# Kernel optimization log

Measured on AMD Instinct MI355X. Metric: run time of the kernel, lower is better.

The kernel has to match this reference:

```python
import jax, jax.numpy as jnp
from jax import lax
import numpy as np
import math

D = 256; H = 4; DH = 64; PERIOD = 30; WIN = 4; L = 2
AUDIO = 768; MOTION = 33
B = 8; T = 1024; S = 1024


def _pe_table(t, d=D, period=PERIOD):
    pos = np.arange(period, dtype=np.float32)[:, None]
    div = np.exp(np.arange(0, d, 2, dtype=np.float32) * (-math.log(10000.0) / d))
    pe = np.zeros((period, d), np.float32)
    pe[:, 0::2] = np.sin(pos * div)
    pe[:, 1::2] = np.cos(pos * div)
    reps = t // period + 1
    return jnp.asarray(np.tile(pe, (reps, 1))[:t])


def _tgt_mask(t):
    # ALiBi-style bias (quantized by period) + causal mask, per head. [H,t,t]
    slopes = jnp.array([0.25 ** (i + 1) for i in range(H)], jnp.float32)
    i = jnp.arange(t)[:, None]
    j = jnp.arange(t)[None, :]
    rel = i - j
    alibi = jnp.where(rel >= 0, -(rel // PERIOD).astype(jnp.float32), 0.0)
    causal = jnp.where(rel >= 0, 0.0, -jnp.inf)
    return slopes[:, None, None] * alibi + causal[None]


def _mem_mask(t, s):
    i = jnp.arange(t)[:, None]
    j = jnp.arange(s)[None, :]
    return jnp.where(jnp.abs(i - j) <= WIN, 0.0, -jnp.inf)


def _ln(x, g, b, eps=1e-5):
    mu = jnp.mean(x, -1, keepdims=True)
    var = jnp.mean(jnp.square(x - mu), -1, keepdims=True)
    return (x - mu) * lax.rsqrt(var + eps) * g + b


def _mha(xq, xkv, in_w, in_b, out_w, out_b, mask):
    wq, wk, wv = jnp.split(in_w, 3, axis=0)
    bq, bk, bv = jnp.split(in_b, 3)
    q = xq @ wq.T + bq
    k = xkv @ wk.T + bk
    v = xkv @ wv.T + bv
    b_, t_, _ = q.shape
    s_ = k.shape[1]
    q = q.reshape(b_, t_, H, DH)
    k = k.reshape(b_, s_, H, DH)
    v = v.reshape(b_, s_, H, DH)
    scores = jnp.einsum('bthd,bshd->bhts', q, k) / math.sqrt(DH) + mask
    a = jax.nn.softmax(scores, axis=-1)
    o = jnp.einsum('bhts,bshd->bthd', a, v).reshape(b_, t_, D)
    return o @ out_w.T + out_b


def _conv1d(x_nch, w, b):
    y = lax.conv_general_dilated(x_nch, w, (1,), [(2, 2)],
                                 dimension_numbers=('NCH', 'OIH', 'NCH'))
    return y + b[None, :, None]


def setup_inputs() -> dict:
    key = jax.random.key(0)
    ks = iter(jax.random.split(key, 40))

    def r(shape, s=0.05):
        return jax.random.normal(next(ks), shape, jnp.float32) * s

    return {
        'hidden_states': jax.random.normal(next(ks), (B, S, AUDIO), jnp.float32),
        'target_motions': jax.random.uniform(next(ks), (B, T, MOTION), jnp.float32),
        'W_af': r((D, AUDIO)), 'b_af': r((D,)),
        'conv1_w': r((D, D, 5)), 'conv1_b': r((D,)),
        'conv2_w': r((D, D, 5)), 'conv2_b': r((D,)),
        'W_vm': r((D, MOTION)), 'b_vm': r((D,)),
        'sa_in_w': r((L, 3 * D, D)), 'sa_in_b': r((L, 3 * D)),
        'sa_out_w': r((L, D, D)), 'sa_out_b': r((L, D)),
        'ca_in_w': r((L, 3 * D, D)), 'ca_in_b': r((L, 3 * D)),
        'ca_out_w': r((L, D, D)), 'ca_out_b': r((L, D)),
        'ln1_g': jnp.ones((L, D)), 'ln1_b': jnp.zeros((L, D)),
        'ln2_g': jnp.ones((L, D)), 'ln2_b': jnp.zeros((L, D)),
        'ln3_g': jnp.ones((L, D)), 'ln3_b': jnp.zeros((L, D)),
        'ff1_w': r((L, 2 * D, D)), 'ff1_b': r((L, 2 * D)),
        'ff2_w': r((L, D, 2 * D)), 'ff2_b': r((L, D)),
        'W_vr': r((MOTION, D)), 'b_vr': r((MOTION,)),
    }


def reference(hidden_states, target_motions, W_af, b_af, conv1_w, conv1_b,
              conv2_w, conv2_b, W_vm, b_vm, sa_in_w, sa_in_b, sa_out_w,
              sa_out_b, ca_in_w, ca_in_b, ca_out_w, ca_out_b, ln1_g, ln1_b,
              ln2_g, ln2_b, ln3_g, ln3_b, ff1_w, ff1_b, ff2_w, ff2_b,
              W_vr, b_vr):
    # audio encoder: linear + residual temporal convs (exact GELU)
    audio = hidden_states @ W_af.T + b_af                       # [B,S,D]
    c = _conv1d(audio.transpose(0, 2, 1), conv1_w, conv1_b)
    c = jax.nn.gelu(c, approximate=False)
    c = _conv1d(c, conv2_w, conv2_b)
    audio = audio + c.transpose(0, 2, 1)

    b_, t_, _ = target_motions.shape
    motion_in = jnp.concatenate(
        [jnp.zeros((b_, 1, MOTION), target_motions.dtype),
         target_motions[:, :-1]], axis=1)
    x = motion_in @ W_vm.T + b_vm + _pe_table(t_)               # PPE (eval: no dropout)

    tm = _tgt_mask(t_)                                          # [H,t,t]
    mm = _mem_mask(t_, audio.shape[1])                          # [t,s]

    for l in range(L):  # post-norm TransformerDecoderLayer, relu FFN
        x = _ln(x + _mha(x, x, sa_in_w[l], sa_in_b[l], sa_out_w[l], sa_out_b[l], tm),
                ln1_g[l], ln1_b[l])
        x = _ln(x + _mha(x, audio, ca_in_w[l], ca_in_b[l], ca_out_w[l], ca_out_b[l], mm),
                ln2_g[l], ln2_b[l])
        h = jax.nn.relu(x @ ff1_w[l].T + ff1_b[l]) @ ff2_w[l].T + ff2_b[l]
        x = _ln(x + h, ln3_g[l], ln3_b[l])

    return jnp.clip(x @ W_vr.T + b_vr, 0.0, 1.0)
```

## Files before the change

kernel.cpp:

```cpp
#include <hip/hip_runtime.h>
#include <math.h>

#define B_ 8
#define T_ 1024
#define S_ 1024
#define D_ 256
#define H_ 4
#define DH_ 64
#define AUDIO_ 768
#define MOTION_ 33
#define PERIOD_ 30
#define WIN_ 4
#define M_ (B_ * T_)

typedef _Float16 half8 __attribute__((ext_vector_type(8)));
typedef _Float16 half4 __attribute__((ext_vector_type(4)));
typedef __attribute__((ext_vector_type(4))) float f32x4;

#define O_AF    0
#define O_SAIN  196608
#define O_SAOUT 589824
#define O_CAIN  720896
#define O_CAOUT 1114112
#define O_FF1   1245184
#define O_FF2   1507328
#define O_CONV1 1769472
#define O_CONV2 2097152
#define O_VR    2424832
#define WH_TOT  2441216
#define HID_TOT 6291456

struct CvtSrc { const float* p[17]; };

__global__ __launch_bounds__(256) void cvt_all(
    CvtSrc s, _Float16* __restrict__ wH, _Float16* __restrict__ hidH) {
  const long i = (long)blockIdx.x * 256 + threadIdx.x;
  if (i >= (long)WH_TOT + HID_TOT) return;
  if (i >= WH_TOT) { const long j = i - WH_TOT; hidH[j] = (_Float16)s.p[15][j]; return; }
  if (i >= O_VR) {
    const long j = i - O_VR, oc = j >> 8, cin = j & 255;
    wH[i] = (oc < MOTION_) ? (_Float16)s.p[16][oc * 256 + cin] : (_Float16)0.f;
    return;
  }
  if (i >= O_CONV2) {
    const long j = i - O_CONV2, oc = j / 1280, r = j % 1280, tap = r >> 8, cin = r & 255;
    wH[i] = (_Float16)s.p[14][(oc * 256 + cin) * 5 + tap]; return;
  }
  if (i >= O_CONV1) {
    const long j = i - O_CONV1, oc = j / 1280, r = j % 1280, tap = r >> 8, cin = r & 255;
    wH[i] = (_Float16)s.p[13][(oc * 256 + cin) * 5 + tap]; return;
  }
  int seg; long base;
  if      (i >= 1638400) { seg = 12; base = 1638400; }
  else if (i >= 1507328) { seg = 11; base = 1507328; }
  else if (i >= 1376256) { seg = 10; base = 1376256; }
  else if (i >= 1245184) { seg = 9;  base = 1245184; }
  else if (i >= 1179648) { seg = 8;  base = 1179648; }
  else if (i >= 1114112) { seg = 7;  base = 1114112; }
  else if (i >= 917504)  { seg = 6;  base = 917504; }
  else if (i >= 720896)  { seg = 5;  base = 720896; }
  else if (i >= 655360)  { seg = 4;  base = 655360; }
  else if (i >= 589824)  { seg = 3;  base = 589824; }
  else if (i >= 393216)  { seg = 2;  base = 393216; }
  else if (i >= 196608)  { seg = 1;  base = 196608; }
  else                   { seg = 0;  base = 0; }
  wH[i] = (_Float16)s.p[seg][i - base];
}

__global__ __launch_bounds__(256) void gemm_h(
    const _Float16* __restrict__ A, const _Float16* __restrict__ W,
    const float* __restrict__ bias, float* __restrict__ Cf,
    _Float16* __restrict__ Ch, int M, int N, int K, int relu) {
  __shared__ _Float16 As[64][72];
  __shared__ _Float16 Bs[64][72];
  const int tid = threadIdx.x;
  const int wave = tid >> 6, lane = tid & 63;
  const int wr = wave >> 1, wc = wave & 1;
  const int lr16 = lane & 15, kq = lane >> 4;
  const int bm = blockIdx.x, bn = blockIdx.y;
  const int sr = tid >> 2, sq = tid & 3;

  const _Float16* Ap = A + (size_t)(bm * 64 + sr) * K + sq * 8;
  const _Float16* Wp = W + (size_t)(bn * 64 + sr) * K + sq * 8;

  half8 ra0 = *reinterpret_cast<const half8*>(Ap);
  half8 ra1 = *reinterpret_cast<const half8*>(Ap + 32);
  half8 rw0 = *reinterpret_cast<const half8*>(Wp);
  half8 rw1 = *reinterpret_cast<const half8*>(Wp + 32);
  f32x4 acc[2][2] = {};

  for (int k0 = 0; k0 < K; k0 += 64) {
    __syncthreads();
    *reinterpret_cast<half8*>(&As[sr][sq * 8]) = ra0;
    *reinterpret_cast<half8*>(&As[sr][32 + sq * 8]) = ra1;
    *reinterpret_cast<half8*>(&Bs[sr][sq * 8]) = rw0;
    *reinterpret_cast<half8*>(&Bs[sr][32 + sq * 8]) = rw1;
    __syncthreads();
    if (k0 + 64 < K) {
      ra0 = *reinterpret_cast<const half8*>(Ap + k0 + 64);
      ra1 = *reinterpret_cast<const half8*>(Ap + k0 + 96);
      rw0 = *reinterpret_cast<const half8*>(Wp + k0 + 64);
      rw1 = *reinterpret_cast<const half8*>(Wp + k0 + 96);
    }
    half8 af[2][2], bf[2][2];
#pragma unroll
    for (int m = 0; m < 2; ++m)
#pragma unroll
      for (int s = 0; s < 2; ++s)
        af[m][s] = *reinterpret_cast<const half8*>(
            &As[wr * 32 + m * 16 + lr16][s * 32 + kq * 8]);
#pragma unroll
    for (int n = 0; n < 2; ++n)
#pragma unroll
      for (int s = 0; s < 2; ++s)
        bf[n][s] = *reinterpret_cast<const half8*>(
            &Bs[wc * 32 + n * 16 + lr16][s * 32 + kq * 8]);
#pragma unroll
    for (int m = 0; m < 2; ++m)
#pragma unroll
      for (int n = 0; n < 2; ++n)
#pragma unroll
        for (int s = 0; s < 2; ++s)
          acc[m][n] = __builtin_amdgcn_mfma_f32_16x16x32_f16(af[m][s], bf[n][s], acc[m][n], 0, 0, 0);
  }

#pragma unroll
  for (int m = 0; m < 2; ++m) {
#pragma unroll
    for (int n = 0; n < 2; ++n) {
      const int col = bn * 64 + wc * 32 + n * 16 + lr16;
      const float bv = bias[col];
#pragma unroll
      for (int j = 0; j < 4; ++j) {
        const int row = bm * 64 + wr * 32 + m * 16 + kq * 4 + j;
        float v = acc[m][n][j] + bv;
        if (relu) v = fmaxf(v, 0.f);
        const size_t idx = (size_t)row * N + col;
        if (Cf) Cf[idx] = v;
        if (Ch) Ch[idx] = (_Float16)v;
      }
    }
  }
}

__device__ __forceinline__ half8 conv_ld(const _Float16* Xb, int p, int tap, int cin) {
  const int sp = p + tap - 2;
  if (sp < 0 || sp >= S_) { half8 z = {}; return z; }
  return *reinterpret_cast<const half8*>(Xb + (size_t)sp * D_ + cin);
}

__global__ __launch_bounds__(256) void conv_h(
    const _Float16* __restrict__ Xh, const _Float16* __restrict__ Wc,
    const float* __restrict__ bias, _Float16* __restrict__ OutH,
    const float* __restrict__ ResF, int mode) {
  __shared__ _Float16 As[64][72];
  __shared__ _Float16 Bs[64][72];
  const int tid = threadIdx.x;
  const int wave = tid >> 6, lane = tid & 63;
  const int wr = wave >> 1, wc = wave & 1;
  const int lr16 = lane & 15, kq = lane >> 4;
  const int b = blockIdx.x >> 4;
  const int s0 = (blockIdx.x & 15) * 64;
  const int o0 = blockIdx.y * 64;
  const int sr = tid >> 2, sq = tid & 3;

  const _Float16* Xb = Xh + (size_t)b * S_ * D_;
  const _Float16* Wp = Wc + (size_t)(o0 + sr) * 1280 + sq * 8;
  const int p = s0 + sr;

  half8 ra0 = conv_ld(Xb, p, 0, sq * 8);
  half8 ra1 = conv_ld(Xb, p, 0, 32 + sq * 8);
  half8 rw0 = *reinterpret_cast<const half8*>(Wp);
  half8 rw1 = *reinterpret_cast<const half8*>(Wp + 32);
  f32x4 acc[2][2] = {};

  for (int k0 = 0; k0 < 1280; k0 += 64) {
    __syncthreads();
    *reinterpret_cast<half8*>(&As[sr][sq * 8]) = ra0;
    *reinterpret_cast<half8*>(&As[sr][32 + sq * 8]) = ra1;
    *reinterpret_cast<half8*>(&Bs[sr][sq * 8]) = rw0;
    *reinterpret_cast<half8*>(&Bs[sr][32 + sq * 8]) = rw1;
    __syncthreads();
    if (k0 + 64 < 1280) {
      const int kn = k0 + 64;
      const int tap = kn >> 8, cb = kn & 255;
      ra0 = conv_ld(Xb, p, tap, cb + sq * 8);
      ra1 = conv_ld(Xb, p, tap, cb + 32 + sq * 8);
      rw0 = *reinterpret_cast<const half8*>(Wp + kn);
      rw1 = *reinterpret_cast<const half8*>(Wp + kn + 32);
    }
    half8 af[2][2], bf[2][2];
#pragma unroll
    for (int m = 0; m < 2; ++m)
#pragma unroll
      for (int s = 0; s < 2; ++s)
        af[m][s] = *reinterpret_cast<const half8*>(
            &As[wr * 32 + m * 16 + lr16][s * 32 + kq * 8]);
#pragma unroll
    for (int n = 0; n < 2; ++n)
#pragma unroll
      for (int s = 0; s < 2; ++s)
        bf[n][s] = *reinterpret_cast<const half8*>(
            &Bs[wc * 32 + n * 16 + lr16][s * 32 + kq * 8]);
#pragma unroll
    for (int m = 0; m < 2; ++m)
#pragma unroll
      for (int n = 0; n < 2; ++n)
#pragma unroll
        for (int s = 0; s < 2; ++s)
          acc[m][n] = __builtin_amdgcn_mfma_f32_16x16x32_f16(af[m][s], bf[n][s], acc[m][n], 0, 0, 0);
  }

#pragma unroll
  for (int m = 0; m < 2; ++m) {
#pragma unroll
    for (int n = 0; n < 2; ++n) {
      const int oc = o0 + wc * 32 + n * 16 + lr16;
      const float bv = bias[oc];
#pragma unroll
      for (int j = 0; j < 4; ++j) {
        const int s = s0 + wr * 32 + m * 16 + kq * 4 + j;
        const size_t idx = ((size_t)b * S_ + s) * D_ + oc;
        float v = acc[m][n][j] + bv;
        if (mode == 0) {
          v = 0.5f * v * (1.f + erff(v * 0.70710678118654752f));
        } else {
          v += ResF[idx];
        }
        OutH[idx] = (_Float16)v;
      }
    }
  }
}

__global__ __launch_bounds__(256) void head_mfma(
    const _Float16* __restrict__ Xh, const _Float16* __restrict__ Wh,
    const float* __restrict__ bv, float* __restrict__ Out) {
  __shared__ _Float16 As[64][72];
  __shared__ _Float16 Bs[64][72];
  const int tid = threadIdx.x;
  const int wave = tid >> 6, lane = tid & 63;
  const int wr = wave >> 1, wc = wave & 1;
  const int lr16 = lane & 15, kq = lane >> 4;
  const int bm = blockIdx.x;
  const int sr = tid >> 2, sq = tid & 3;

  const _Float16* Ap = Xh + (size_t)(bm * 64 + sr) * D_ + sq * 8;
  const _Float16* Wp = Wh + (size_t)sr * D_ + sq * 8;

  half8 ra0 = *reinterpret_cast<const half8*>(Ap);
  half8 ra1 = *reinterpret_cast<const half8*>(Ap + 32);
  half8 rw0 = *reinterpret_cast<const half8*>(Wp);
  half8 rw1 = *reinterpret_cast<const half8*>(Wp + 32);
  f32x4 acc[2][2] = {};

  for (int k0 = 0; k0 < D_; k0 += 64) {
    __syncthreads();
    *reinterpret_cast<half8*>(&As[sr][sq * 8]) = ra0;
    *reinterpret_cast<half8*>(&As[sr][32 + sq * 8]) = ra1;
    *reinterpret_cast<half8*>(&Bs[sr][sq * 8]) = rw0;
    *reinterpret_cast<half8*>(&Bs[sr][32 + sq * 8]) = rw1;
    __syncthreads();
    if (k0 + 64 < D_) {
      ra0 = *reinterpret_cast<const half8*>(Ap + k0 + 64);
      ra1 = *reinterpret_cast<const half8*>(Ap + k0 + 96);
      rw0 = *reinterpret_cast<const half8*>(Wp + k0 + 64);
      rw1 = *reinterpret_cast<const half8*>(Wp + k0 + 96);
    }
    half8 af[2][2], bf[2][2];
#pragma unroll
    for (int m = 0; m < 2; ++m)
#pragma unroll
      for (int s = 0; s < 2; ++s)
        af[m][s] = *reinterpret_cast<const half8*>(
            &As[wr * 32 + m * 16 + lr16][s * 32 + kq * 8]);
#pragma unroll
    for (int n = 0; n < 2; ++n)
#pragma unroll
      for (int s = 0; s < 2; ++s)
        bf[n][s] = *reinterpret_cast<const half8*>(
            &Bs[wc * 32 + n * 16 + lr16][s * 32 + kq * 8]);
#pragma unroll
    for (int m = 0; m < 2; ++m)
#pragma unroll
      for (int n = 0; n < 2; ++n)
#pragma unroll
        for (int s = 0; s < 2; ++s)
          acc[m][n] = __builtin_amdgcn_mfma_f32_16x16x32_f16(af[m][s], bf[n][s], acc[m][n], 0, 0, 0);
  }

#pragma unroll
  for (int m = 0; m < 2; ++m) {
#pragma unroll
    for (int n = 0; n < 2; ++n) {
      const int col = wc * 32 + n * 16 + lr16;
      if (col < MOTION_) {
        const float bb = bv[col];
#pragma unroll
        for (int j = 0; j < 4; ++j) {
          const int row = bm * 64 + wr * 32 + m * 16 + kq * 4 + j;
          float v = acc[m][n][j] + bb;
          Out[(size_t)row * MOTION_ + col] = fminf(fmaxf(v, 0.f), 1.f);
        }
      }
    }
  }
}

__global__ __launch_bounds__(256) void motion_pe(
    const float* __restrict__ TM, const float* __restrict__ Wvm,
    const float* __restrict__ bvm, float* __restrict__ Xout,
    _Float16* __restrict__ XoutH) {
  const int d = threadIdx.x;
  const int bt = blockIdx.x;
  const int t = bt & (T_ - 1);
  const int b = bt >> 10;
  float acc = bvm[d];
  if (t > 0) {
    const float* mrow = TM + ((size_t)b * T_ + t - 1) * MOTION_;
    const float* wrow = Wvm + (size_t)d * MOTION_;
#pragma unroll
    for (int m = 0; m < MOTION_; ++m) acc += mrow[m] * wrow[m];
  }
  const int pos = t % PERIOD_;
  const int i2 = d >> 1;
  const float div = expf((float)(2 * i2) * (-9.210340371976184f / 256.f));
  const float ang = (float)pos * div;
  acc += (d & 1) ? cosf(ang) : sinf(ang);
  Xout[(size_t)bt * D_ + d] = acc;
  XoutH[(size_t)bt * D_ + d] = (_Float16)acc;
}

#define RS_ 72
__global__ __launch_bounds__(512) void self_attn(
    const _Float16* __restrict__ QKV, _Float16* __restrict__ O) {
  __shared__ _Float16 Ks[64 * RS_];
  __shared__ _Float16 VTs[64 * RS_];
  __shared__ _Float16 Ps[8][16 * RS_];
  const int qtb = blockIdx.x, h = blockIdx.y, b = blockIdx.z;
  const int tid = threadIdx.x;
  const int wave = tid >> 6, lane = tid & 63;
  const int lo = lane & 15, hi = lane >> 4;
  const float slope = exp2f(-2.f * (float)(h + 1));
  const int qloc = wave * 16 + lo;
  const int tq = qtb * 128 + qloc;
  const size_t base = (size_t)b * T_ * 768 + h * 64;

  half8 qf[2];
#pragma unroll
  for (int s = 0; s < 2; ++s)
    qf[s] = *reinterpret_cast<const half8*>(
        QKV + base + (size_t)(qtb * 128 + qloc) * 768 + s * 32 + hi * 8);

  f32x4 oacc[4] = {};
  float mrun = -1e30f, lrun = 0.f;

  const int nkt = 2 * qtb + 2;
  for (int kt = 0; kt < nkt; ++kt) {
    __syncthreads();
    {
      const int j = tid >> 3, ch = tid & 7;
      const size_t rowoff = base + (size_t)(kt * 64 + j) * 768;
      *reinterpret_cast<half8*>(&Ks[j * RS_ + ch * 8]) =
          *reinterpret_cast<const half8*>(QKV + rowoff + 256 + ch * 8);
      const half8 vv = *reinterpret_cast<const half8*>(QKV + rowoff + 512 + ch * 8);
#pragma unroll
      for (int r = 0; r < 8; ++r) {
        const int d = ch * 8 + r;
        const int sw = ((d & 7) ^ (d >> 3)) << 3;
        VTs[d * RS_ + (j ^ sw)] = vv[r];
      }
    }
    __syncthreads();

    f32x4 st[4] = {};
#pragma unroll
    for (int f = 0; f < 4; ++f) {
#pragma unroll
      for (int s = 0; s < 2; ++s) {
        const half8 kf = *reinterpret_cast<const half8*>(
            &Ks[(f * 16 + lo) * RS_ + s * 32 + hi * 8]);
        st[f] = __builtin_amdgcn_mfma_f32_16x16x32_f16(kf, qf[s], st[f], 0, 0, 0);
      }
    }

    float sc[4][4];
    float tmax = -1e30f;
#pragma unroll
    for (int f = 0; f < 4; ++f)
#pragma unroll
      for (int r = 0; r < 4; ++r) {
        const int j = kt * 64 + f * 16 + hi * 4 + r;
        const int rel = tq - j;
        const float v = (rel >= 0)
            ? st[f][r] * 0.125f - slope * (float)(rel / PERIOD_) : -1e30f;
        sc[f][r] = v;
        tmax = fmaxf(tmax, v);
      }
    tmax = fmaxf(tmax, __shfl_xor(tmax, 16, 64));
    tmax = fmaxf(tmax, __shfl_xor(tmax, 32, 64));
    const float mnew = fmaxf(mrun, tmax);
    const float scale = __expf(mrun - mnew);

    float psum = 0.f;
#pragma unroll
    for (int f = 0; f < 4; ++f) {
      half4 ph;
#pragma unroll
      for (int r = 0; r < 4; ++r) {
        const float pv = __expf(sc[f][r] - mnew);
        psum += pv;
        ph[r] = (_Float16)pv;
      }
      *reinterpret_cast<half4*>(&Ps[wave][lo * RS_ + f * 16 + hi * 4]) = ph;
    }
    psum += __shfl_xor(psum, 16, 64);
    psum += __shfl_xor(psum, 32, 64);
    lrun = lrun * scale + psum;
    mrun = mnew;

    float rsc[4];
#pragma unroll
    for (int r = 0; r < 4; ++r) rsc[r] = __shfl(scale, hi * 4 + r, 64);
#pragma unroll
    for (int nf = 0; nf < 4; ++nf)
#pragma unroll
      for (int r = 0; r < 4; ++r) oacc[nf][r] *= rsc[r];

#pragma unroll
    for (int s = 0; s < 2; ++s) {
      const half8 pf = *reinterpret_cast<const half8*>(
          &Ps[wave][lo * RS_ + s * 32 + hi * 8]);
#pragma unroll
      for (int nf = 0; nf < 4; ++nf) {
        const int d = nf * 16 + lo;
        const int sw = ((d & 7) ^ (d >> 3)) << 3;
        const half8 vf = *reinterpret_cast<const half8*>(
            &VTs[d * RS_ + ((s * 32 + hi * 8) ^ sw)]);
        oacc[nf] = __builtin_amdgcn_mfma_f32_16x16x32_f16(pf, vf, oacc[nf], 0, 0, 0);
      }
    }
  }

  float invl[4];
#pragma unroll
  for (int r = 0; r < 4; ++r) invl[r] = 1.f / __shfl(lrun, hi * 4 + r, 64);
#pragma unroll
  for (int nf = 0; nf < 4; ++nf)
#pragma unroll
    for (int r = 0; r < 4; ++r) {
      const int q = qtb * 128 + wave * 16 + hi * 4 + r;
      O[((size_t)b * T_ + q) * D_ + h * 64 + nf * 16 + lo] =
          (_Float16)(oacc[nf][r] * invl[r]);
    }
}

__global__ __launch_bounds__(256) void cross_attn(
    const _Float16* __restrict__ Q, const _Float16* __restrict__ KV,
    _Float16* __restrict__ O) {
  const int gid = blockIdx.x * 256 + threadIdx.x;
  const int h = gid & 3;
  const int bt = gid >> 2;
  const int t = bt & (T_ - 1);
  const int b = bt >> 10;

  float q[64];
  const _Float16* qp = Q + (size_t)bt * D_ + h * 64;
#pragma unroll
  for (int d0 = 0; d0 < 64; d0 += 8) {
    const half8 v = *reinterpret_cast<const half8*>(qp + d0);
#pragma unroll
    for (int e = 0; e < 8; ++e) q[d0 + e] = (float)v[e];
  }

  const int j0 = (t - WIN_ > 0) ? t - WIN_ : 0;
  const int j1 = (t + WIN_ < S_ - 1) ? t + WIN_ : S_ - 1;
  const int nj = j1 - j0 + 1;

  float sc[9];
  float mx = -1e30f;
#pragma unroll
  for (int jj = 0; jj < 9; ++jj) {
    if (jj < nj) {
      const _Float16* kp = KV + ((size_t)b * S_ + j0 + jj) * 512 + h * 64;
      float s = 0.f;
#pragma unroll
      for (int d0 = 0; d0 < 64; d0 += 8) {
        const half8 kv = *reinterpret_cast<const half8*>(kp + d0);
#pragma unroll
        for (int e = 0; e < 8; ++e) s += q[d0 + e] * (float)kv[e];
      }
      sc[jj] = s * 0.125f;
      mx = fmaxf(mx, sc[jj]);
    } else {
      sc[jj] = -1e30f;
    }
  }
  float l = 0.f;
  float p[9];
#pragma unroll
  for (int jj = 0; jj < 9; ++jj) { p[jj] = __expf(sc[jj] - mx); l += p[jj]; }
  const float inv = 1.f / l;

  float o[64];
#pragma unroll
  for (int d = 0; d < 64; ++d) o[d] = 0.f;
#pragma unroll
  for (int jj = 0; jj < 9; ++jj) {
    if (jj < nj) {
      const float pj = p[jj] * inv;
      const _Float16* vp = KV + ((size_t)b * S_ + j0 + jj) * 512 + 256 + h * 64;
#pragma unroll
      for (int d0 = 0; d0 < 64; d0 += 8) {
        const half8 vv = *reinterpret_cast<const half8*>(vp + d0);
#pragma unroll
        for (int e = 0; e < 8; ++e) o[d0 + e] += pj * (float)vv[e];
      }
    }
  }
  _Float16* op = O + (size_t)bt * D_ + h * 64;
#pragma unroll
  for (int d = 0; d < 64; ++d) op[d] = (_Float16)o[d];
}

__global__ __launch_bounds__(256) void ln_res(
    const float* X, const float* __restrict__ R,
    const float* __restrict__ g, const float* __restrict__ bta,
    float* Out, _Float16* __restrict__ OutH) {
  const int wid = threadIdx.x >> 6, lane = threadIdx.x & 63;
  const size_t row = (size_t)blockIdx.x * 4 + wid;
  const float* xp = X + row * D_;
  const float* rp = R + row * D_;
  float v[4];
  float s = 0.f;
#pragma unroll
  for (int k = 0; k < 4; ++k) {
    const int d = lane + k * 64;
    v[k] = xp[d] + rp[d];
    s += v[k];
  }
#pragma unroll
  for (int off = 32; off; off >>= 1) s += __shfl_xor(s, off, 64);
  const float mu = s * (1.f / 256.f);
  float var = 0.f;
#pragma unroll
  for (int k = 0; k < 4; ++k) { const float d = v[k] - mu; var += d * d; }
#pragma unroll
  for (int off = 32; off; off >>= 1) var += __shfl_xor(var, off, 64);
  const float rs = rsqrtf(var * (1.f / 256.f) + 1e-5f);
#pragma unroll
  for (int k = 0; k < 4; ++k) {
    const int d = lane + k * 64;
    const float o = (v[k] - mu) * rs * g[d] + bta[d];
    Out[row * D_ + d] = o;
    OutH[row * D_ + d] = (_Float16)o;
  }
}

extern "C" void kernel_launch(void* const* d_in, const int* in_sizes, int n_in,
                              void* d_out, int out_size, void* d_ws, size_t ws_size,
                              hipStream_t stream) {
  (void)in_sizes; (void)n_in; (void)out_size; (void)ws_size;
  const float* hidden = (const float*)d_in[0];
  const float* tmot   = (const float*)d_in[1];
  const float* W_af   = (const float*)d_in[2];
  const float* b_af   = (const float*)d_in[3];
  const float* c1w    = (const float*)d_in[4];
  const float* c1b    = (const float*)d_in[5];
  const float* c2w    = (const float*)d_in[6];
  const float* c2b    = (const float*)d_in[7];
  const float* Wvm    = (const float*)d_in[8];
  const float* bvm    = (const float*)d_in[9];
  const float* sa_in_w  = (const float*)d_in[10];
  const float* sa_in_b  = (const float*)d_in[11];
  const float* sa_out_w = (const float*)d_in[12];
  const float* sa_out_b = (const float*)d_in[13];
  const float* ca_in_w  = (const float*)d_in[14];
  const float* ca_in_b  = (const float*)d_in[15];
  const float* ca_out_w = (const float*)d_in[16];
  const float* ca_out_b = (const float*)d_in[17];
  const float* ln1g = (const float*)d_in[18];
  const float* ln1b = (const float*)d_in[19];
  const float* ln2g = (const float*)d_in[20];
  const float* ln2b = (const float*)d_in[21];
  const float* ln3g = (const float*)d_in[22];
  const float* ln3b = (const float*)d_in[23];
  const float* ff1w = (const float*)d_in[24];
  const float* ff1b = (const float*)d_in[25];
  const float* ff2w = (const float*)d_in[26];
  const float* ff2b = (const float*)d_in[27];
  const float* Wvr  = (const float*)d_in[28];
  const float* bvr  = (const float*)d_in[29];
  float* out = (float*)d_out;

  float* ws = (float*)d_ws;
  const size_t BSD = (size_t)M_ * D_;
  float* audio = ws;
  float* x     = ws + BSD;
  float* t1    = ws + 2 * BSD;
  _Float16* hb = (_Float16*)(ws + 3 * BSD);
  _Float16* Rh      = hb;
  _Float16* x_h     = hb + 3 * BSD;
  _Float16* audio_h = hb + 4 * BSD;
  _Float16* att_h   = hb + 5 * BSD;
  _Float16* wH      = hb + 6 * BSD;
  _Float16* ckv_h   = Rh + BSD;

  const dim3 blk(256);

  CvtSrc cs;
  cs.p[0] = W_af;
  cs.p[1] = sa_in_w;            cs.p[2] = sa_in_w + 768 * 256;
  cs.p[3] = sa_out_w;           cs.p[4] = sa_out_w + 256 * 256;
  cs.p[5] = ca_in_w;            cs.p[6] = ca_in_w + 768 * 256;
  cs.p[7] = ca_out_w;           cs.p[8] = ca_out_w + 256 * 256;
  cs.p[9] = ff1w;               cs.p[10] = ff1w + 512 * 256;
  cs.p[11] = ff2w;              cs.p[12] = ff2w + 256 * 512;
  cs.p[13] = c1w;               cs.p[14] = c2w;
  cs.p[15] = hidden;            cs.p[16] = Wvr;
  cvt_all<<<dim3((WH_TOT + HID_TOT + 255) / 256), blk, 0, stream>>>(cs, wH, Rh);

  gemm_h<<<dim3(M_ / 64, 4), blk, 0, stream>>>(Rh, wH + O_AF, b_af, audio, audio_h,
                                               M_, 256, 768, 0);
  conv_h<<<dim3(128, 4), blk, 0, stream>>>(audio_h, wH + O_CONV1, c1b, Rh, nullptr, 0);
  conv_h<<<dim3(128, 4), blk, 0, stream>>>(Rh, wH + O_CONV2, c2b, audio_h, audio, 1);

  motion_pe<<<dim3(M_), blk, 0, stream>>>(tmot, Wvm, bvm, x, x_h);

  for (int l = 0; l < 2; ++l) {
    gemm_h<<<dim3(M_ / 64, 12), blk, 0, stream>>>(
        x_h, wH + O_SAIN + l * 196608, sa_in_b + l * 768, nullptr, Rh, M_, 768, 256, 0);
    self_attn<<<dim3(T_ / 128, H_, B_), dim3(512), 0, stream>>>(Rh, att_h);
    gemm_h<<<dim3(M_ / 64, 4), blk, 0, stream>>>(
        att_h, wH + O_SAOUT + l * 65536, sa_out_b + l * 256, t1, nullptr, M_, 256, 256, 0);
    ln_res<<<dim3(M_ / 4), blk, 0, stream>>>(x, t1, ln1g + l * 256, ln1b + l * 256, x, x_h);

    gemm_h<<<dim3(M_ / 64, 4), blk, 0, stream>>>(
        x_h, wH + O_CAIN + l * 196608, ca_in_b + l * 768, nullptr, Rh, M_, 256, 256, 0);
    gemm_h<<<dim3(M_ / 64, 8), blk, 0, stream>>>(
        audio_h, wH + O_CAIN + l * 196608 + 65536, ca_in_b + l * 768 + 256,
        nullptr, ckv_h, M_, 512, 256, 0);
    cross_attn<<<dim3(M_ * H_ / 256), blk, 0, stream>>>(Rh, ckv_h, att_h);
    gemm_h<<<dim3(M_ / 64, 4), blk, 0, stream>>>(
        att_h, wH + O_CAOUT + l * 65536, ca_out_b + l * 256, t1, nullptr, M_, 256, 256, 0);
    ln_res<<<dim3(M_ / 4), blk, 0, stream>>>(x, t1, ln2g + l * 256, ln2b + l * 256, x, x_h);

    gemm_h<<<dim3(M_ / 64, 8), blk, 0, stream>>>(
        x_h, wH + O_FF1 + l * 131072, ff1b + l * 512, nullptr, Rh, M_, 512, 256, 1);
    gemm_h<<<dim3(M_ / 64, 4), blk, 0, stream>>>(
        Rh, wH + O_FF2 + l * 131072, ff2b + l * 256, t1, nullptr, M_, 256, 512, 0);
    ln_res<<<dim3(M_ / 4), blk, 0, stream>>>(x, t1, ln3g + l * 256, ln3b + l * 256, x, x_h);
  }

  head_mfma<<<dim3(M_ / 64), blk, 0, stream>>>(x_h, wH + O_VR, bvr, out);
}
```

Baseline: 365.9 us.

## Double-buffer K/V tiles in self-attention with register prefetch

The self-attention kernel now loads the next K/V tile from global memory into registers before computing on the current tile. It then writes that tile into a second shared-memory buffer after the PV MFMAs, which halves the barriers per iteration and hides global load latency behind compute. The transposed-V buffer also drops its padding (stride 64) and relies on the existing XOR swizzle to avoid bank conflicts. The cost is more LDS, which may affect occupancy, and extra live registers for the prefetched data.

```diff
diff --git a/kernel.cpp b/kernel.cpp
--- a/kernel.cpp
+++ b/kernel.cpp
@@ -331,12 +331,13 @@
   XoutH[(size_t)bt * D_ + d] = (_Float16)acc;
 }
 
-#define RS_ 72
+#define RSK_ 72
+#define RSV_ 64
 __global__ __launch_bounds__(512) void self_attn(
     const _Float16* __restrict__ QKV, _Float16* __restrict__ O) {
-  __shared__ _Float16 Ks[64 * RS_];
-  __shared__ _Float16 VTs[64 * RS_];
-  __shared__ _Float16 Ps[8][16 * RS_];
+  __shared__ _Float16 Ks[2][64 * RSK_];
+  __shared__ _Float16 VTs[2][64 * RSV_];
+  __shared__ _Float16 Ps[8][16 * RSK_];
   const int qtb = blockIdx.x, h = blockIdx.y, b = blockIdx.z;
   const int tid = threadIdx.x;
   const int wave = tid >> 6, lane = tid & 63;
@@ -345,6 +346,7 @@
   const int qloc = wave * 16 + lo;
   const int tq = qtb * 128 + qloc;
   const size_t base = (size_t)b * T_ * 768 + h * 64;
+  const int sj = tid >> 3, sch = tid & 7;
 
   half8 qf[2];
 #pragma unroll
@@ -356,22 +358,30 @@
   float mrun = -1e30f, lrun = 0.f;
 
   const int nkt = 2 * qtb + 2;
+
+  half8 rk, rv;
+  {
+    const size_t rowoff = base + (size_t)sj * 768;
+    rk = *reinterpret_cast<const half8*>(QKV + rowoff + 256 + sch * 8);
+    rv = *reinterpret_cast<const half8*>(QKV + rowoff + 512 + sch * 8);
+    *reinterpret_cast<half8*>(&Ks[0][sj * RSK_ + sch * 8]) = rk;
+#pragma unroll
+    for (int r = 0; r < 8; ++r) {
+      const int d = sch * 8 + r;
+      const int sw = ((d & 7) ^ (d >> 3)) << 3;
+      VTs[0][d * RSV_ + (sj ^ sw)] = rv[r];
+    }
+  }
+  __syncthreads();
+
   for (int kt = 0; kt < nkt; ++kt) {
-    __syncthreads();
-    {
-      const int j = tid >> 3, ch = tid & 7;
-      const size_t rowoff = base + (size_t)(kt * 64 + j) * 768;
-      *reinterpret_cast<half8*>(&Ks[j * RS_ + ch * 8]) =
-          *reinterpret_cast<const half8*>(QKV + rowoff + 256 + ch * 8);
-      const half8 vv = *reinterpret_cast<const half8*>(QKV + rowoff + 512 + ch * 8);
-#pragma unroll
-      for (int r = 0; r < 8; ++r) {
-        const int d = ch * 8 + r;
-        const int sw = ((d & 7) ^ (d >> 3)) << 3;
-        VTs[d * RS_ + (j ^ sw)] = vv[r];
-      }
-    }
-    __syncthreads();
+    const int cur = kt & 1;
+    const bool more = (kt + 1 < nkt);
+    if (more) {
+      const size_t rowoff = base + (size_t)((kt + 1) * 64 + sj) * 768;
+      rk = *reinterpret_cast<const half8*>(QKV + rowoff + 256 + sch * 8);
+      rv = *reinterpret_cast<const half8*>(QKV + rowoff + 512 + sch * 8);
+    }
 
     f32x4 st[4] = {};
 #pragma unroll
@@ -379,7 +389,7 @@
 #pragma unroll
       for (int s = 0; s < 2; ++s) {
         const half8 kf = *reinterpret_cast<const half8*>(
-            &Ks[(f * 16 + lo) * RS_ + s * 32 + hi * 8]);
+            &Ks[cur][(f * 16 + lo) * RSK_ + s * 32 + hi * 8]);
         st[f] = __builtin_amdgcn_mfma_f32_16x16x32_f16(kf, qf[s], st[f], 0, 0, 0);
       }
     }
@@ -412,7 +422,7 @@
         psum += pv;
         ph[r] = (_Float16)pv;
       }
-      *reinterpret_cast<half4*>(&Ps[wave][lo * RS_ + f * 16 + hi * 4]) = ph;
+      *reinterpret_cast<half4*>(&Ps[wave][lo * RSK_ + f * 16 + hi * 4]) = ph;
     }
     psum += __shfl_xor(psum, 16, 64);
     psum += __shfl_xor(psum, 32, 64);
@@ -430,15 +440,26 @@
 #pragma unroll
     for (int s = 0; s < 2; ++s) {
       const half8 pf = *reinterpret_cast<const half8*>(
-          &Ps[wave][lo * RS_ + s * 32 + hi * 8]);
+          &Ps[wave][lo * RSK_ + s * 32 + hi * 8]);
 #pragma unroll
       for (int nf = 0; nf < 4; ++nf) {
         const int d = nf * 16 + lo;
         const int sw = ((d & 7) ^ (d >> 3)) << 3;
         const half8 vf = *reinterpret_cast<const half8*>(
-            &VTs[d * RS_ + ((s * 32 + hi * 8) ^ sw)]);
+            &VTs[cur][d * RSV_ + ((s * 32 + hi * 8) ^ sw)]);
         oacc[nf] = __builtin_amdgcn_mfma_f32_16x16x32_f16(pf, vf, oacc[nf], 0, 0, 0);
       }
+    }
+
+    if (more) {
+      *reinterpret_cast<half8*>(&Ks[cur ^ 1][sj * RSK_ + sch * 8]) = rk;
+#pragma unroll
+      for (int r = 0; r < 8; ++r) {
+        const int d = sch * 8 + r;
+        const int sw = ((d & 7) ^ (d >> 3)) << 3;
+        VTs[cur ^ 1][d * RSV_ + (sj ^ sw)] = rv[r];
+      }
+      __syncthreads();
     }
   }
 
```

Result: no change. 359.8 us (-1.7%).
